# Kernel tuning notes

Hardware: AMD Instinct MI355X
Metric: run time of the kernel (lower is better)

The kernel has to match this reference:

```python
import jax, jax.numpy as jnp
import numpy as np

N = 4096      # nodes
E = 131072    # edges (before self loops)
C = 512       # channels
H = 8         # heads
CO = C // H   # per-head out channels (64)
EPS = 1e-5
NEG_SLOPE = 0.2


def layer_norm(x, g, b):
    mu = jnp.mean(x, axis=-1, keepdims=True)
    var = jnp.mean((x - mu) ** 2, axis=-1, keepdims=True)
    return (x - mu) * jax.lax.rsqrt(var + EPS) * g + b


def gatv2(x, src, dst, wl, bl, wr, br, att, bias):
    # PyG GATv2Conv, concat=True, add_self_loops handled by caller.
    n = x.shape[0]
    xl = (x @ wl.T + bl).reshape(n, H, CO)   # target-side features
    xr = (x @ wr.T + br).reshape(n, H, CO)   # source-side features (messages)
    e = jax.nn.leaky_relu(xl[dst] + xr[src], NEG_SLOPE)   # [E+N, H, CO]
    alpha = jnp.einsum('ehc,hc->eh', e, att)              # [E+N, H]
    # segment softmax over destination neighborhoods
    amax = jax.ops.segment_max(alpha, dst, num_segments=n)
    ex = jnp.exp(alpha - amax[dst])
    denom = jax.ops.segment_sum(ex, dst, num_segments=n)
    a = ex / denom[dst]                                   # [E+N, H]
    msg = xr[src] * a[:, :, None]                         # [E+N, H, CO]
    out = jax.ops.segment_sum(msg, dst, num_segments=n)   # [N, H, CO]
    return out.reshape(n, H * CO) + bias


def mha(x, in_w, in_b, out_w, out_b):
    # nn.MultiheadAttention self-attention, batch=1, eval mode
    n = x.shape[0]
    qkv = x @ in_w.T + in_b                               # [N, 3C]
    q, k, v = jnp.split(qkv, 3, axis=-1)
    q = q.reshape(n, H, CO); k = k.reshape(n, H, CO); v = v.reshape(n, H, CO)
    scores = jnp.einsum('qhd,khd->hqk', q, k) / jnp.sqrt(jnp.float32(CO))
    p = jax.nn.softmax(scores, axis=-1)
    o = jnp.einsum('hqk,khd->qhd', p, v).reshape(n, C)
    return o @ out_w.T + out_b


def setup_inputs() -> dict:
    key = jax.random.key(0)
    ks = jax.random.split(key, 24)
    s = 0.02
    d = {}
    d['x'] = jax.random.normal(ks[0], (N, C), jnp.float32)
    d['edge_index'] = jax.random.randint(ks[1], (2, E), 0, N, dtype=jnp.int64)
    d['gat_wl'] = jax.random.normal(ks[2], (H * CO, C), jnp.float32) * s
    d['gat_bl'] = jnp.zeros((H * CO,), jnp.float32)
    d['gat_wr'] = jax.random.normal(ks[3], (H * CO, C), jnp.float32) * s
    d['gat_br'] = jnp.zeros((H * CO,), jnp.float32)
    d['gat_att'] = jax.random.normal(ks[4], (H, CO), jnp.float32) * s
    d['gat_b'] = jnp.zeros((H * CO,), jnp.float32)
    d['in_w'] = jax.random.normal(ks[5], (3 * C, C), jnp.float32) * s
    d['in_b'] = jnp.zeros((3 * C,), jnp.float32)
    d['out_w'] = jax.random.normal(ks[6], (C, C), jnp.float32) * s
    d['out_b'] = jnp.zeros((C,), jnp.float32)
    d['ln1_g'] = jnp.ones((C,), jnp.float32); d['ln1_b'] = jnp.zeros((C,), jnp.float32)
    d['ln2_g'] = jnp.ones((C,), jnp.float32); d['ln2_b'] = jnp.zeros((C,), jnp.float32)
    d['ln3_g'] = jnp.ones((C,), jnp.float32); d['ln3_b'] = jnp.zeros((C,), jnp.float32)
    d['w1'] = jax.random.normal(ks[7], (4 * C, C), jnp.float32) * s
    d['b1'] = jnp.zeros((4 * C,), jnp.float32)
    d['w2'] = jax.random.normal(ks[8], (C, 4 * C), jnp.float32) * s
    d['b2'] = jnp.zeros((C,), jnp.float32)
    return d


def reference(x, edge_index, gat_wl, gat_bl, gat_wr, gat_br, gat_att, gat_b,
              in_w, in_b, out_w, out_b, ln1_g, ln1_b, ln2_g, ln2_b,
              ln3_g, ln3_b, w1, b1, w2, b2):
    n = x.shape[0]
    loops = jnp.arange(n, dtype=edge_index.dtype)
    src = jnp.concatenate([edge_index[0], loops])
    dst = jnp.concatenate([edge_index[1], loops])
    h_local = gatv2(x, src, dst, gat_wl, gat_bl, gat_wr, gat_br, gat_att, gat_b)
    x = layer_norm(x + h_local, ln1_g, ln1_b)
    h_global = mha(x, in_w, in_b, out_w, out_b)
    x = layer_norm(x + h_global, ln2_g, ln2_b)
    h_ffn = (jax.nn.gelu(x @ w1.T + b1, approximate=False)) @ w2.T + b2
    x = layer_norm(x + h_ffn, ln3_g, ln3_b)
    return x
```

## Files before the change

kernel.cpp:

```cpp
#include <hip/hip_runtime.h>
#include <math.h>

#define NN 4096
#define CC 512
#define EE 131072
#define NEDGE (EE + NN)
#define HH 8
#define DCO 64
#define NC2 2097152L

typedef __attribute__((ext_vector_type(8))) short bfrag;
typedef __attribute__((ext_vector_type(4))) float f32x4;
typedef __attribute__((ext_vector_type(4))) int i32x4;

__device__ __forceinline__ float bf2f(unsigned short u) {
  union { float f; unsigned int i; } x; x.i = ((unsigned int)u) << 16; return x.f;
}
__device__ __forceinline__ unsigned short f2bf(float f) {
  union { float f; unsigned int i; } x; x.f = f;
  unsigned int r = x.i + 0x7FFFu + ((x.i >> 16) & 1u);
  return (unsigned short)(r >> 16);
}
__device__ __forceinline__ unsigned short f2bf_trunc(float f) {
  union { float f; unsigned int i; } x; x.f = f;
  return (unsigned short)(x.i >> 16);
}

__device__ __forceinline__ void gld16(const unsigned short* g, unsigned short* l) {
  __builtin_amdgcn_global_load_lds(
      (__attribute__((address_space(1))) unsigned int*)g,
      (__attribute__((address_space(3))) unsigned int*)l, 16, 0, 0);
}

#define QSC 0.18033688011112042f

#define CX  2097152L
#define CWL (CX + 262144L)
#define CWR (CWL + 262144L)
#define CIW (CWR + 786432L)
#define COW (CIW + 262144L)
#define CW1 (COW + 1048576L)
#define CW2 (CW1 + 1048576L)

__global__ void cvt_all(const float* __restrict__ x, const float* __restrict__ wl,
                        const float* __restrict__ wr, const float* __restrict__ iw,
                        const float* __restrict__ ow, const float* __restrict__ w1,
                        const float* __restrict__ w2, unsigned short* __restrict__ dst) {
  long i = ((long)blockIdx.x * 256 + threadIdx.x) * 4;
  if (i >= CW2) return;
  const float* s; long o;
  if (i < CX)       { s = x;  o = i; }
  else if (i < CWL) { s = wl; o = i - CX; }
  else if (i < CWR) { s = wr; o = i - CWL; }
  else if (i < CIW) { s = iw; o = i - CWR; }
  else if (i < COW) { s = ow; o = i - CIW; }
  else if (i < CW1) { s = w1; o = i - COW; }
  else              { s = w2; o = i - CW1; }
  f32x4 v = *(const f32x4*)(s + o);
  union { unsigned long long q; unsigned short u[4]; } t;
#pragma unroll
  for (int j = 0; j < 4; j++) t.u[j] = f2bf(v[j]);
  *(unsigned long long*)(dst + i) = t.q;
}

template<int OMODE, int TN, bool SPLIT>
__global__ __launch_bounds__(256) void gemm_t(
    const unsigned short* __restrict__ A, const unsigned short* __restrict__ B,
    const float* __restrict__ bias, void* __restrict__ C,
    int K, int lda, int ldb, int ldc)
{
  __shared__ unsigned short As[4096];
  __shared__ unsigned short Bs[TN * 32];
  constexpr int MI = (TN == 128) ? 4 : 2;
  const int tid = threadIdx.x;
  const int wave = tid >> 6, lane = tid & 63;
  const int ml = lane & 15, kq = lane >> 4;
  const int wm = (TN == 128) ? ((wave >> 1) << 6) : (wave << 5);
  const int wn = (TN == 128) ? ((wave & 1) << 6) : 0;
  const int bm = blockIdx.y << 7, bn = blockIdx.x * TN;
  const int srow = tid >> 2, scol = (tid & 3) << 3;
  if (SPLIT) { A += (long)blockIdx.z * K; B += (long)blockIdx.z * K; }
  const float* biasp = (!SPLIT || blockIdx.z == 0) ? bias : nullptr;
  const unsigned short* Ag = A + (long)(bm + srow) * lda + scol;
  const unsigned short* Bg = B + (long)(bn + srow) * ldb + scol;
  const long astep = (long)64 * lda, bstep = (long)64 * ldb;
  unsigned short* lA0 = As + tid * 8;
  unsigned short* lA1 = As + 2048 + tid * 8;
  unsigned short* lB0 = Bs + tid * 8;
  f32x4 acc[MI][4];
#pragma unroll
  for (int mi = 0; mi < MI; mi++)
#pragma unroll
    for (int ni = 0; ni < 4; ni++) acc[mi][ni] = (f32x4){0.f, 0.f, 0.f, 0.f};
  for (int k0 = 0; k0 < K; k0 += 32) {
    __syncthreads();
    gld16(Ag, lA0); gld16(Ag + astep, lA1);
    gld16(Bg, lB0);
    if (TN == 128) gld16(Bg + bstep, Bs + 2048 + tid * 8);
    Ag += 32; Bg += 32;
    __syncthreads();
    bfrag af[MI], bf[4];
#pragma unroll
    for (int mi = 0; mi < MI; mi++)
      af[mi] = *(const bfrag*)&As[(wm + (mi << 4) + ml) * 32 + (kq << 3)];
#pragma unroll
    for (int ni = 0; ni < 4; ni++)
      bf[ni] = *(const bfrag*)&Bs[(wn + (ni << 4) + ml) * 32 + (kq << 3)];
#pragma unroll
    for (int mi = 0; mi < MI; mi++)
#pragma unroll
      for (int ni = 0; ni < 4; ni++)
        acc[mi][ni] = __builtin_amdgcn_mfma_f32_16x16x32_bf16(af[mi], bf[ni], acc[mi][ni], 0, 0, 0);
  }
#pragma unroll
  for (int ni = 0; ni < 4; ni++) {
    int col = bn + wn + (ni << 4) + ml;
    float bb = biasp ? biasp[col] : 0.f;
#pragma unroll
    for (int mi = 0; mi < MI; mi++) {
      int row0 = bm + wm + (mi << 4) + (kq << 2);
#pragma unroll
      for (int r = 0; r < 4; r++) {
        float v = acc[mi][ni][r] + bb;
        int row = row0 + r;
        if (OMODE == 3) {
          unsigned short* q = (unsigned short*)C;
          if (col < 512) {
            int h = col >> 6, d = col & 63;
            q[(long)h * (NN * DCO) + (long)row * DCO + d] = f2bf(v * QSC);
          } else if (col < 1024) {
            int c2 = col - 512, h = c2 >> 6, d = c2 & 63;
            q[NC2 + (long)h * (NN * DCO) + (long)row * DCO + d] = f2bf(v);
          } else {
            int c2 = col - 1024, h = c2 >> 6, d = c2 & 63;
            q[2 * NC2 + (long)h * (DCO * NN) + (long)d * NN + row] = f2bf(v);
          }
        } else if (OMODE == 0) {
          long off = (SPLIT ? (long)blockIdx.z * NC2 : 0) + (long)row * ldc + col;
          ((float*)C)[off] = v;
        } else {
          if (OMODE == 2) v = 0.5f * v * (1.f + erff(v * 0.70710678118f));
          ((unsigned short*)C)[(long)row * ldc + col] = f2bf(v);
        }
      }
    }
  }
}

__global__ void count_k(const int* __restrict__ ei, int* __restrict__ cnt) {
  int e = blockIdx.x * 256 + threadIdx.x;
  if (e >= NEDGE) return;
  int d = (e < EE) ? ei[EE + e] : (e - EE);
  atomicAdd(&cnt[d], 1);
}

__global__ void scan_k(const int* __restrict__ cnt, int* __restrict__ rowptr) {
  __shared__ int s[1024];
  int t = threadIdx.x;
  int b = t * 4;
  int c0 = cnt[b], c1 = cnt[b + 1], c2 = cnt[b + 2], c3 = cnt[b + 3];
  int sum = c0 + c1 + c2 + c3;
  s[t] = sum;
  __syncthreads();
  for (int o = 1; o < 1024; o <<= 1) {
    int v = (t >= o) ? s[t - o] : 0;
    __syncthreads();
    s[t] += v;
    __syncthreads();
  }
  int ex = s[t] - sum;
  rowptr[b] = ex; rowptr[b + 1] = ex + c0;
  rowptr[b + 2] = ex + c0 + c1; rowptr[b + 3] = ex + c0 + c1 + c2;
  if (t == 1023) rowptr[4096] = ex + sum;
}

__global__ void scatter_k(const int* __restrict__ ei, const int* __restrict__ rowptr,
                          int* __restrict__ cur, int* __restrict__ order) {
  int e = blockIdx.x * 256 + threadIdx.x;
  if (e >= NEDGE) return;
  int d = (e < EE) ? ei[EE + e] : (e - EE);
  int p = atomicAdd(&cur[d], 1);
  order[rowptr[d] + p] = e;
}

__global__ __launch_bounds__(256) void gat_alpha(
    const unsigned short* __restrict__ xlr, const int* __restrict__ order,
    const int* __restrict__ ei, const float* __restrict__ att,
    float* __restrict__ alpha)
{
  int i = (blockIdx.x << 2) + (threadIdx.x >> 6);
  int e = order[i];
  int lane = threadIdx.x & 63;
  int src, dst;
  if (e < EE) { src = ei[e]; dst = ei[EE + e]; } else { src = dst = e - EE; }
  int c = lane << 3;
  union { i32x4 v; unsigned short u[8]; } L, R;
  L.v = *(const i32x4*)(xlr + (long)dst * 1024 + c);
  R.v = *(const i32x4*)(xlr + (long)src * 1024 + 512 + c);
  f32x4 t0 = *(const f32x4*)(att + c);
  f32x4 t1 = *(const f32x4*)(att + c + 4);
  float p = 0.f;
#pragma unroll
  for (int j = 0; j < 8; j++) {
    float x = bf2f(L.u[j]) + bf2f(R.u[j]);
    x = (x > 0.f) ? x : 0.2f * x;
    float tv = (j < 4) ? t0[j] : t1[j - 4];
    p += tv * x;
  }
  p += __shfl_xor(p, 1); p += __shfl_xor(p, 2); p += __shfl_xor(p, 4);
  if ((lane & 7) == 0) alpha[(long)i * 8 + (lane >> 3)] = p;
}

__global__ __launch_bounds__(256) void gat_aggr(
    const unsigned short* __restrict__ xlr, float* __restrict__ alpha,
    const int* __restrict__ order, const int* __restrict__ rowptr,
    const int* __restrict__ ei, const float* __restrict__ gbias,
    float* __restrict__ out)
{
  __shared__ float red[256];
  __shared__ float smax[8], sinv[8];
  __shared__ float part[4][512];
  int n = blockIdx.x, t = threadIdx.x;
  int beg = rowptr[n], deg = rowptr[n + 1] - beg;
  int h8 = t & 7, grp = t >> 3;
  float m = -1e30f;
  for (int i = grp; i < deg; i += 32)
    m = fmaxf(m, alpha[(long)(beg + i) * 8 + h8]);
  red[t] = m; __syncthreads();
  for (int off = 128; off >= 8; off >>= 1) {
    if (t < off) red[t] = fmaxf(red[t], red[t + off]);
    __syncthreads();
  }
  if (t < 8) smax[t] = red[t];
  __syncthreads();
  float mh = smax[h8];
  float s = 0.f;
  for (int i = grp; i < deg; i += 32) {
    long idx = (long)(beg + i) * 8 + h8;
    float ex = __expf(alpha[idx] - mh);
    alpha[idx] = ex;
    s += ex;
  }
  red[t] = s; __syncthreads();
  for (int off = 128; off >= 8; off >>= 1) {
    if (t < off) red[t] += red[t + off];
    __syncthreads();
  }
  if (t < 8) sinv[t] = 1.f / red[t];
  __syncthreads();
  int wave = t >> 6, lane = t & 63;
  int ch = lane << 3;
  int hh = lane >> 3;
  float acc[8];
#pragma unroll
  for (int j = 0; j < 8; j++) acc[j] = 0.f;
  for (int i = wave; i < deg; i += 4) {
    int e = order[beg + i];
    int sn = (e < EE) ? ei[e] : (e - EE);
    float wgt = alpha[(long)(beg + i) * 8 + hh];
    union { i32x4 v; unsigned short u[8]; } X;
    X.v = *(const i32x4*)(xlr + (long)sn * 1024 + 512 + ch);
#pragma unroll
    for (int j = 0; j < 8; j++) acc[j] += wgt * bf2f(X.u[j]);
  }
  *(f32x4*)&part[wave][ch]     = (f32x4){acc[0], acc[1], acc[2], acc[3]};
  *(f32x4*)&part[wave][ch + 4] = (f32x4){acc[4], acc[5], acc[6], acc[7]};
  __syncthreads();
#pragma unroll
  for (int c = t; c < 512; c += 256) {
    float v = part[0][c] + part[1][c] + part[2][c] + part[3][c];
    out[(long)n * CC + c] = v * sinv[c >> 6] + gbias[c];
  }
}

template<bool SUM2>
__global__ __launch_bounds__(256) void resid_ln(
    const float* __restrict__ a, const float* __restrict__ b,
    const float* __restrict__ g, const float* __restrict__ be,
    float* __restrict__ of, unsigned short* __restrict__ ob)
{
  __shared__ float sh[8];
  int row = blockIdx.x, t = threadIdx.x;
  long base = (long)row * CC;
  float b0 = b[base + t], b1 = b[base + t + 256];
  if (SUM2) { b0 += b[NC2 + base + t]; b1 += b[NC2 + base + t + 256]; }
  float v0 = a[base + t] + b0;
  float v1 = a[base + t + 256] + b1;
  float s = v0 + v1, ss = v0 * v0 + v1 * v1;
  for (int o = 32; o > 0; o >>= 1) { s += __shfl_down(s, o); ss += __shfl_down(ss, o); }
  int wave = t >> 6, lane = t & 63;
  if (lane == 0) { sh[wave] = s; sh[4 + wave] = ss; }
  __syncthreads();
  float S = sh[0] + sh[1] + sh[2] + sh[3];
  float SS = sh[4] + sh[5] + sh[6] + sh[7];
  float mean = S * (1.f / 512.f);
  float var = SS * (1.f / 512.f) - mean * mean;
  float rs = rsqrtf(var + 1e-5f);
  float y0 = (v0 - mean) * rs * g[t] + be[t];
  float y1 = (v1 - mean) * rs * g[t + 256] + be[t + 256];
  if (of) { of[base + t] = y0; of[base + t + 256] = y1; }
  if (ob) { ob[base + t] = f2bf(y0); ob[base + t + 256] = f2bf(y1); }
}

__global__ __launch_bounds__(256, 4) void flash_attn(
    const unsigned short* __restrict__ qkvP, unsigned short* __restrict__ Op,
    float* __restrict__ Lp)
{
  __shared__ unsigned short QP[128 * 72];
  __shared__ unsigned short Ks[64 * 72];
  __shared__ unsigned short Vs[64 * 72];
  const int tid = threadIdx.x;
  const int wave = tid >> 6, lane = tid & 63;
  const int ml = lane & 15, kq = lane >> 4;
  const int h = blockIdx.x & 7, qt = blockIdx.x >> 3;
  const int sp = blockIdx.y;
  const int n0 = qt << 7;
  const unsigned short* Qh = qkvP + (long)h * (NN * DCO);
  const unsigned short* Kh = qkvP + NC2 + (long)h * (NN * DCO);
  const unsigned short* Vh = qkvP + 2 * NC2 + (long)h * (DCO * NN);
  {
    int r = tid >> 1, c = (tid & 1) << 5;
    const unsigned short* src = Qh + (long)(n0 + r) * DCO + c;
    unsigned short* d = &QP[r * 72 + c];
    *(i32x4*)d        = *(const i32x4*)src;
    *(i32x4*)(d + 8)  = *(const i32x4*)(src + 8);
    *(i32x4*)(d + 16) = *(const i32x4*)(src + 16);
    *(i32x4*)(d + 24) = *(const i32x4*)(src + 24);
  }
  __syncthreads();
  bfrag aq[2][2];
#pragma unroll
  for (int s = 0; s < 2; s++)
#pragma unroll
    for (int kh = 0; kh < 2; kh++)
      aq[s][kh] = *(const bfrag*)&QP[(wave * 32 + s * 16 + ml) * 72 + kh * 32 + (kq << 3)];
  bfrag ones;
#pragma unroll
  for (int j = 0; j < 8; j++) ones[j] = (short)0x3F80;
  f32x4 Oa[2][4];
  f32x4 Lc[2];
#pragma unroll
  for (int s = 0; s < 2; s++) {
    Lc[s] = (f32x4){0.f, 0.f, 0.f, 0.f};
#pragma unroll
    for (int dg = 0; dg < 4; dg++) Oa[s][dg] = (f32x4){0.f, 0.f, 0.f, 0.f};
  }
  const int r_ = tid >> 2, c_ = (tid & 3) << 4;
  const int j0 = sp << 4;
  i32x4 ka, kb, va, vb;
  {
    int k0 = j0 << 6;
    ka = *(const i32x4*)(Kh + (long)(k0 + r_) * DCO + c_);
    kb = *(const i32x4*)(Kh + (long)(k0 + r_) * DCO + c_ + 8);
    va = *(const i32x4*)(Vh + (long)r_ * NN + k0 + c_);
    vb = *(const i32x4*)(Vh + (long)r_ * NN + k0 + c_ + 8);
  }
  for (int jj = 0; jj < 16; jj++) {
    if (jj) __syncthreads();
    *(i32x4*)&Ks[r_ * 72 + c_] = ka; *(i32x4*)&Ks[r_ * 72 + c_ + 8] = kb;
    *(i32x4*)&Vs[r_ * 72 + c_] = va; *(i32x4*)&Vs[r_ * 72 + c_ + 8] = vb;
    __syncthreads();
    if (jj < 15) {
      int k0 = (j0 + jj + 1) << 6;
      ka = *(const i32x4*)(Kh + (long)(k0 + r_) * DCO + c_);
      kb = *(const i32x4*)(Kh + (long)(k0 + r_) * DCO + c_ + 8);
      va = *(const i32x4*)(Vh + (long)r_ * NN + k0 + c_);
      vb = *(const i32x4*)(Vh + (long)r_ * NN + k0 + c_ + 8);
    }
    f32x4 sc[2][4];
#pragma unroll
    for (int s = 0; s < 2; s++)
#pragma unroll
      for (int c = 0; c < 4; c++) sc[s][c] = (f32x4){0.f, 0.f, 0.f, 0.f};
#pragma unroll
    for (int c = 0; c < 4; c++) {
      bfrag bk0 = *(const bfrag*)&Ks[(c * 16 + ml) * 72 + (kq << 3)];
      bfrag bk1 = *(const bfrag*)&Ks[(c * 16 + ml) * 72 + 32 + (kq << 3)];
#pragma unroll
      for (int s = 0; s < 2; s++) {
        sc[s][c] = __builtin_amdgcn_mfma_f32_16x16x32_bf16(aq[s][0], bk0, sc[s][c], 0, 0, 0);
        sc[s][c] = __builtin_amdgcn_mfma_f32_16x16x32_bf16(aq[s][1], bk1, sc[s][c], 0, 0, 0);
      }
    }
#pragma unroll
    for (int s = 0; s < 2; s++)
#pragma unroll
      for (int c = 0; c < 4; c++)
#pragma unroll
        for (int r = 0; r < 4; r++) {
          float p = exp2f(sc[s][c][r]);
          QP[(wave * 32 + s * 16 + (kq << 2) + r) * 72 + c * 16 + ml] = f2bf_trunc(p);
        }
    bfrag ap[2][2];
#pragma unroll
    for (int s = 0; s < 2; s++)
#pragma unroll
      for (int kh = 0; kh < 2; kh++)
        ap[s][kh] = *(const bfrag*)&QP[(wave * 32 + s * 16 + ml) * 72 + kh * 32 + (kq << 3)];
#pragma unroll
    for (int s = 0; s < 2; s++) {
      Lc[s] = __builtin_amdgcn_mfma_f32_16x16x32_bf16(ap[s][0], ones, Lc[s], 0, 0, 0);
      Lc[s] = __builtin_amdgcn_mfma_f32_16x16x32_bf16(ap[s][1], ones, Lc[s], 0, 0, 0);
    }
#pragma unroll
    for (int dg = 0; dg < 4; dg++) {
      bfrag bv0 = *(const bfrag*)&Vs[(dg * 16 + ml) * 72 + (kq << 3)];
      bfrag bv1 = *(const bfrag*)&Vs[(dg * 16 + ml) * 72 + 32 + (kq << 3)];
#pragma unroll
      for (int s = 0; s < 2; s++) {
        Oa[s][dg] = __builtin_amdgcn_mfma_f32_16x16x32_bf16(ap[s][0], bv0, Oa[s][dg], 0, 0, 0);
        Oa[s][dg] = __builtin_amdgcn_mfma_f32_16x16x32_bf16(ap[s][1], bv1, Oa[s][dg], 0, 0, 0);
      }
    }
  }
  long obase = (long)sp * NC2;
#pragma unroll
  for (int s = 0; s < 2; s++)
#pragma unroll
    for (int dg = 0; dg < 4; dg++)
#pragma unroll
      for (int r = 0; r < 4; r++) {
        int row = wave * 32 + s * 16 + (kq << 2) + r;
        Op[obase + (long)(n0 + row) * CC + (h << 6) + (dg << 4) + ml] = f2bf(Oa[s][dg][r]);
      }
  if (ml == 0) {
#pragma unroll
    for (int s = 0; s < 2; s++)
#pragma unroll
      for (int r = 0; r < 4; r++) {
        int row = wave * 32 + s * 16 + (kq << 2) + r;
        Lp[(long)sp * (NN * HH) + (long)(n0 + row) * HH + h] = Lc[s][r];
      }
  }
}

__global__ void flash_combine(const unsigned short* __restrict__ Op,
                              const float* __restrict__ Lp,
                              unsigned short* __restrict__ Ao) {
  int idx = blockIdx.x * 256 + threadIdx.x;
  int n = idx >> 9, c = idx & 511, h = c >> 6;
  float l = 0.f, o = 0.f;
#pragma unroll
  for (int s = 0; s < 4; s++) {
    l += Lp[(long)s * (NN * HH) + (long)n * HH + h];
    o += bf2f(Op[(long)s * NC2 + idx]);
  }
  Ao[idx] = f2bf(o / l);
}

extern "C" void kernel_launch(void* const* d_in, const int* in_sizes, int n_in,
                              void* d_out, int out_size, void* d_ws, size_t ws_size,
                              hipStream_t stream) {
  typedef unsigned short u16;
  const float* x      = (const float*)d_in[0];
  const int*   ei     = (const int*)d_in[1];
  const float* wl     = (const float*)d_in[2];
  const float* bl     = (const float*)d_in[3];
  const float* wr     = (const float*)d_in[4];
  const float* br     = (const float*)d_in[5];
  const float* att    = (const float*)d_in[6];
  const float* gat_b  = (const float*)d_in[7];
  const float* in_w   = (const float*)d_in[8];
  const float* in_b   = (const float*)d_in[9];
  const float* out_w  = (const float*)d_in[10];
  const float* out_b  = (const float*)d_in[11];
  const float* ln1g   = (const float*)d_in[12];
  const float* ln1b   = (const float*)d_in[13];
  const float* ln2g   = (const float*)d_in[14];
  const float* ln2b   = (const float*)d_in[15];
  const float* ln3g   = (const float*)d_in[16];
  const float* ln3b   = (const float*)d_in[17];
  const float* w1     = (const float*)d_in[18];
  const float* b1     = (const float*)d_in[19];
  const float* w2     = (const float*)d_in[20];
  const float* b2     = (const float*)d_in[21];

  const size_t MB = 1u << 20;
  char* w = (char*)d_ws;
  float* h_f32   = (float*)(w + 0);
  float* x2_f32  = (float*)(w + 8 * MB);
  int*   cnt     = (int*)(w + 16 * MB);
  int*   rowptr  = (int*)(w + 16 * MB + 32 * 1024);
  int*   order   = (int*)(w + 16 * MB + 64 * 1024);
  u16*   cvt     = (u16*)(w + 17 * MB);
  u16*   xbf     = cvt;
  u16*   wlrbf   = cvt + CX;
  u16*   inwbf   = cvt + CWR;
  u16*   outwbf  = cvt + CIW;
  u16*   w1bf    = cvt + COW;
  u16*   w2bf    = cvt + CW1;
  u16*   xlr_bf  = (u16*)(w + 29 * MB);
  float* alpha   = (float*)(w + 37 * MB);
  float* gat_out = (float*)(w + 42 * MB);
  u16*   Opart   = (u16*)(w + 29 * MB);
  float* proj    = (float*)(w + 29 * MB);
  u16*   ffn1    = (u16*)(w + 45 * MB);
  u16*   qkvP    = (u16*)(w + 93 * MB);
  float* biasc   = (float*)(w + 105 * MB);
  float* Lpart   = (float*)(w + 105 * MB);
  u16*   Ao      = (u16*)(w + 106 * MB);
  u16*   actb    = (u16*)(w + 110 * MB);

  cvt_all<<<5632, 256, 0, stream>>>(x, wl, wr, in_w, out_w, w1, w2, cvt);
  hipMemsetAsync(cnt, 0, NN * sizeof(int), stream);
  count_k<<<(NEDGE + 255) / 256, 256, 0, stream>>>(ei, cnt);
  scan_k<<<1, 1024, 0, stream>>>(cnt, rowptr);
  hipMemsetAsync(cnt, 0, NN * sizeof(int), stream);
  scatter_k<<<(NEDGE + 255) / 256, 256, 0, stream>>>(ei, rowptr, cnt, order);

  hipMemcpyAsync(biasc, bl, 512 * sizeof(float), hipMemcpyDeviceToDevice, stream);
  hipMemcpyAsync(biasc + 512, br, 512 * sizeof(float), hipMemcpyDeviceToDevice, stream);
  gemm_t<1, 64, false><<<dim3(16, 32), 256, 0, stream>>>(xbf, wlrbf, biasc, xlr_bf, 512, 512, 512, 1024);
  gat_alpha<<<NEDGE / 4, 256, 0, stream>>>(xlr_bf, order, ei, att, alpha);
  gat_aggr<<<NN, 256, 0, stream>>>(xlr_bf, alpha, order, rowptr, ei, gat_b, gat_out);
  resid_ln<false><<<NN, 256, 0, stream>>>(x, gat_out, ln1g, ln1b, h_f32, actb);

  gemm_t<3, 64, false><<<dim3(24, 32), 256, 0, stream>>>(actb, inwbf, in_b, qkvP, 512, 512, 512, 0);
  flash_attn<<<dim3(256, 4), 256, 0, stream>>>(qkvP, Opart, Lpart);
  flash_combine<<<(NN * CC) / 256, 256, 0, stream>>>(Opart, Lpart, Ao);
  gemm_t<0, 64, true><<<dim3(8, 32, 2), 256, 0, stream>>>(Ao, outwbf, out_b, proj, 256, 512, 512, 512);
  resid_ln<true><<<NN, 256, 0, stream>>>(h_f32, proj, ln2g, ln2b, x2_f32, actb);

  gemm_t<2, 128, false><<<dim3(16, 32), 256, 0, stream>>>(actb, w1bf, b1, ffn1, 512, 512, 512, 2048);
  gemm_t<0, 64, true><<<dim3(8, 32, 2), 256, 0, stream>>>(ffn1, w2bf, b2, proj, 1024, 2048, 2048, 512);
  resid_ln<true><<<NN, 256, 0, stream>>>(x2_f32, proj, ln3g, ln3b, (float*)d_out, nullptr);
}
```

Measured before the change: 372.8 us.

## Fold memsets and bias copies into cvt kernel; restructure flash attention P handling

The conversion kernel gets two extra blocks that zero both edge-count arrays and copy the GAT biases, replacing two memsets and two device copies. Scatter now uses a separate cursor array so only one zeroing is needed. In flash attention, Q fragments are loaded straight from global memory instead of being staged in LDS. Scores are computed transposed (K as A operand) so each lane packs four P values into one 8-byte LDS store. The row sum is accumulated in registers from the truncated P values and reduced with shuffles, which removes the ones-matrix MFMAs.

```diff
diff --git a/kernel.cpp b/kernel.cpp
--- a/kernel.cpp
+++ b/kernel.cpp
@@ -21,10 +21,6 @@
   unsigned int r = x.i + 0x7FFFu + ((x.i >> 16) & 1u);
   return (unsigned short)(r >> 16);
 }
-__device__ __forceinline__ unsigned short f2bf_trunc(float f) {
-  union { float f; unsigned int i; } x; x.f = f;
-  return (unsigned short)(x.i >> 16);
-}
 
 __device__ __forceinline__ void gld16(const unsigned short* g, unsigned short* l) {
   __builtin_amdgcn_global_load_lds(
@@ -45,9 +41,22 @@
 __global__ void cvt_all(const float* __restrict__ x, const float* __restrict__ wl,
                         const float* __restrict__ wr, const float* __restrict__ iw,
                         const float* __restrict__ ow, const float* __restrict__ w1,
-                        const float* __restrict__ w2, unsigned short* __restrict__ dst) {
+                        const float* __restrict__ w2, unsigned short* __restrict__ dst,
+                        int* __restrict__ cntcur, const float* __restrict__ bl,
+                        const float* __restrict__ br, float* __restrict__ biasc) {
+  if (blockIdx.x >= 5632) {
+    int t = threadIdx.x;
+    if (blockIdx.x == 5632) {
+      for (int k = t; k < 8192; k += 256) cntcur[k] = 0;
+    } else {
+      for (int k = t; k < 512; k += 256) {
+        biasc[k] = bl[k];
+        biasc[512 + k] = br[k];
+      }
+    }
+    return;
+  }
   long i = ((long)blockIdx.x * 256 + threadIdx.x) * 4;
-  if (i >= CW2) return;
   const float* s; long o;
   if (i < CX)       { s = x;  o = i; }
   else if (i < CWL) { s = wl; o = i - CX; }
@@ -306,7 +315,7 @@
     const unsigned short* __restrict__ qkvP, unsigned short* __restrict__ Op,
     float* __restrict__ Lp)
 {
-  __shared__ unsigned short QP[128 * 72];
+  __shared__ unsigned short Ps[128 * 72];
   __shared__ unsigned short Ks[64 * 72];
   __shared__ unsigned short Vs[64 * 72];
   const int tid = threadIdx.x;
@@ -318,33 +327,18 @@
   const unsigned short* Qh = qkvP + (long)h * (NN * DCO);
   const unsigned short* Kh = qkvP + NC2 + (long)h * (NN * DCO);
   const unsigned short* Vh = qkvP + 2 * NC2 + (long)h * (DCO * NN);
-  {
-    int r = tid >> 1, c = (tid & 1) << 5;
-    const unsigned short* src = Qh + (long)(n0 + r) * DCO + c;
-    unsigned short* d = &QP[r * 72 + c];
-    *(i32x4*)d        = *(const i32x4*)src;
-    *(i32x4*)(d + 8)  = *(const i32x4*)(src + 8);
-    *(i32x4*)(d + 16) = *(const i32x4*)(src + 16);
-    *(i32x4*)(d + 24) = *(const i32x4*)(src + 24);
-  }
-  __syncthreads();
   bfrag aq[2][2];
 #pragma unroll
   for (int s = 0; s < 2; s++)
 #pragma unroll
     for (int kh = 0; kh < 2; kh++)
-      aq[s][kh] = *(const bfrag*)&QP[(wave * 32 + s * 16 + ml) * 72 + kh * 32 + (kq << 3)];
-  bfrag ones;
-#pragma unroll
-  for (int j = 0; j < 8; j++) ones[j] = (short)0x3F80;
+      aq[s][kh] = *(const bfrag*)(Qh + (long)(n0 + wave * 32 + s * 16 + ml) * DCO + kh * 32 + (kq << 3));
   f32x4 Oa[2][4];
-  f32x4 Lc[2];
-#pragma unroll
-  for (int s = 0; s < 2; s++) {
-    Lc[s] = (f32x4){0.f, 0.f, 0.f, 0.f};
+  float Lr[2] = {0.f, 0.f};
+#pragma unroll
+  for (int s = 0; s < 2; s++)
 #pragma unroll
     for (int dg = 0; dg < 4; dg++) Oa[s][dg] = (f32x4){0.f, 0.f, 0.f, 0.f};
-  }
   const int r_ = tid >> 2, c_ = (tid & 3) << 4;
   const int j0 = sp << 4;
   i32x4 ka, kb, va, vb;
@@ -367,41 +361,45 @@
       va = *(const i32x4*)(Vh + (long)r_ * NN + k0 + c_);
       vb = *(const i32x4*)(Vh + (long)r_ * NN + k0 + c_ + 8);
     }
-    f32x4 sc[2][4];
+#pragma unroll
+    for (int c = 0; c < 4; c++) {
+      const int krow = (c * 16 + ml) * 72 + (kq << 3);
+      bfrag bk0 = *(const bfrag*)&Ks[krow];
+      bfrag bk1 = *(const bfrag*)&Ks[krow + 32];
+      f32x4 s0 = (f32x4){0.f, 0.f, 0.f, 0.f};
+      f32x4 s1 = (f32x4){0.f, 0.f, 0.f, 0.f};
+      s0 = __builtin_amdgcn_mfma_f32_16x16x32_bf16(bk0, aq[0][0], s0, 0, 0, 0);
+      s0 = __builtin_amdgcn_mfma_f32_16x16x32_bf16(bk1, aq[0][1], s0, 0, 0, 0);
+      s1 = __builtin_amdgcn_mfma_f32_16x16x32_bf16(bk0, aq[1][0], s1, 0, 0, 0);
+      s1 = __builtin_amdgcn_mfma_f32_16x16x32_bf16(bk1, aq[1][1], s1, 0, 0, 0);
+      union { unsigned long long q; unsigned short u[4]; } pk;
+      float ls = 0.f;
+#pragma unroll
+      for (int r = 0; r < 4; r++) {
+        union { float f; unsigned int i; } p; p.f = exp2f(s0[r]);
+        p.i &= 0xFFFF0000u;
+        ls += p.f;
+        pk.u[r] = (unsigned short)(p.i >> 16);
+      }
+      Lr[0] += ls;
+      *(unsigned long long*)&Ps[(wave * 32 + ml) * 72 + c * 16 + (kq << 2)] = pk.q;
+      ls = 0.f;
+#pragma unroll
+      for (int r = 0; r < 4; r++) {
+        union { float f; unsigned int i; } p; p.f = exp2f(s1[r]);
+        p.i &= 0xFFFF0000u;
+        ls += p.f;
+        pk.u[r] = (unsigned short)(p.i >> 16);
+      }
+      Lr[1] += ls;
+      *(unsigned long long*)&Ps[(wave * 32 + 16 + ml) * 72 + c * 16 + (kq << 2)] = pk.q;
+    }
+    bfrag ap[2][2];
 #pragma unroll
     for (int s = 0; s < 2; s++)
 #pragma unroll
-      for (int c = 0; c < 4; c++) sc[s][c] = (f32x4){0.f, 0.f, 0.f, 0.f};
-#pragma unroll
-    for (int c = 0; c < 4; c++) {
-      bfrag bk0 = *(const bfrag*)&Ks[(c * 16 + ml) * 72 + (kq << 3)];
-      bfrag bk1 = *(const bfrag*)&Ks[(c * 16 + ml) * 72 + 32 + (kq << 3)];
-#pragma unroll
-      for (int s = 0; s < 2; s++) {
-        sc[s][c] = __builtin_amdgcn_mfma_f32_16x16x32_bf16(aq[s][0], bk0, sc[s][c], 0, 0, 0);
-        sc[s][c] = __builtin_amdgcn_mfma_f32_16x16x32_bf16(aq[s][1], bk1, sc[s][c], 0, 0, 0);
-      }
-    }
-#pragma unroll
-    for (int s = 0; s < 2; s++)
-#pragma unroll
-      for (int c = 0; c < 4; c++)
-#pragma unroll
-        for (int r = 0; r < 4; r++) {
-          float p = exp2f(sc[s][c][r]);
-          QP[(wave * 32 + s * 16 + (kq << 2) + r) * 72 + c * 16 + ml] = f2bf_trunc(p);
-        }
-    bfrag ap[2][2];
-#pragma unroll
-    for (int s = 0; s < 2; s++)
-#pragma unroll
       for (int kh = 0; kh < 2; kh++)
-        ap[s][kh] = *(const bfrag*)&QP[(wave * 32 + s * 16 + ml) * 72 + kh * 32 + (kq << 3)];
-#pragma unroll
-    for (int s = 0; s < 2; s++) {
-      Lc[s] = __builtin_amdgcn_mfma_f32_16x16x32_bf16(ap[s][0], ones, Lc[s], 0, 0, 0);
-      Lc[s] = __builtin_amdgcn_mfma_f32_16x16x32_bf16(ap[s][1], ones, Lc[s], 0, 0, 0);
-    }
+        ap[s][kh] = *(const bfrag*)&Ps[(wave * 32 + s * 16 + ml) * 72 + kh * 32 + (kq << 3)];
 #pragma unroll
     for (int dg = 0; dg < 4; dg++) {
       bfrag bv0 = *(const bfrag*)&Vs[(dg * 16 + ml) * 72 + (kq << 3)];
@@ -423,14 +421,14 @@
         int row = wave * 32 + s * 16 + (kq << 2) + r;
         Op[obase + (long)(n0 + row) * CC + (h << 6) + (dg << 4) + ml] = f2bf(Oa[s][dg][r]);
       }
-  if (ml == 0) {
-#pragma unroll
-    for (int s = 0; s < 2; s++)
-#pragma unroll
-      for (int r = 0; r < 4; r++) {
-        int row = wave * 32 + s * 16 + (kq << 2) + r;
-        Lp[(long)sp * (NN * HH) + (long)(n0 + row) * HH + h] = Lc[s][r];
-      }
+#pragma unroll
+  for (int s = 0; s < 2; s++) {
+    float l = Lr[s];
+    l += __shfl_xor(l, 16); l += __shfl_xor(l, 32);
+    if (lane < 16) {
+      int row = wave * 32 + s * 16 + lane;
+      Lp[(long)sp * (NN * HH) + (long)(n0 + row) * HH + h] = l;
+    }
   }
 }
 
@@ -480,6 +478,7 @@
   float* h_f32   = (float*)(w + 0);
   float* x2_f32  = (float*)(w + 8 * MB);
   int*   cnt     = (int*)(w + 16 * MB);
+  int*   cur     = cnt + 4096;
   int*   rowptr  = (int*)(w + 16 * MB + 32 * 1024);
   int*   order   = (int*)(w + 16 * MB + 64 * 1024);
   u16*   cvt     = (u16*)(w + 17 * MB);
@@ -501,15 +500,12 @@
   u16*   Ao      = (u16*)(w + 106 * MB);
   u16*   actb    = (u16*)(w + 110 * MB);
 
-  cvt_all<<<5632, 256, 0, stream>>>(x, wl, wr, in_w, out_w, w1, w2, cvt);
-  hipMemsetAsync(cnt, 0, NN * sizeof(int), stream);
+  cvt_all<<<5634, 256, 0, stream>>>(x, wl, wr, in_w, out_w, w1, w2, cvt,
+                                    cnt, bl, br, biasc);
   count_k<<<(NEDGE + 255) / 256, 256, 0, stream>>>(ei, cnt);
   scan_k<<<1, 1024, 0, stream>>>(cnt, rowptr);
-  hipMemsetAsync(cnt, 0, NN * sizeof(int), stream);
-  scatter_k<<<(NEDGE + 255) / 256, 256, 0, stream>>>(ei, rowptr, cnt, order);
-
-  hipMemcpyAsync(biasc, bl, 512 * sizeof(float), hipMemcpyDeviceToDevice, stream);
-  hipMemcpyAsync(biasc + 512, br, 512 * sizeof(float), hipMemcpyDeviceToDevice, stream);
+  scatter_k<<<(NEDGE + 255) / 256, 256, 0, stream>>>(ei, rowptr, cur, order);
+
   gemm_t<1, 64, false><<<dim3(16, 32), 256, 0, stream>>>(xbf, wlrbf, biasc, xlr_bf, 512, 512, 512, 1024);
   gat_alpha<<<NEDGE / 4, 256, 0, stream>>>(xlr_bf, order, ei, att, alpha);
   gat_aggr<<<NN, 256, 0, stream>>>(xlr_bf, alpha, order, rowptr, ei, gat_b, gat_out);
```

New measurement: 364.7 us. 1.02x faster.
